# Kernel tuning notes

Hardware: AMD Instinct MI355X
Metric: run time of the kernel (lower is better)

Reference implementation:

```python
import jax, jax.numpy as jnp
import numpy as np

B, S, H = 1, 2048, 2048
NH, NKV, HD = 16, 2, 128
ROPE_THETA = 1000000.0
BF16 = jnp.bfloat16


def setup_inputs() -> dict:
    key = jax.random.key(0)
    ks = jax.random.split(key, 6)
    hidden_states = jax.random.normal(ks[0], (B, S, H), dtype=jnp.float32)
    # causal additive mask, 0 on/below diagonal, large negative above
    causal = jnp.tril(jnp.ones((S, S), dtype=bool))
    attention_mask = jnp.where(causal, 0.0, -1e9).astype(jnp.float32)[None, None, :, :]
    position_ids = jnp.arange(S, dtype=jnp.int32)[None, :]
    sc = 1.0 / np.sqrt(H)
    Wq = jax.random.normal(ks[1], (H, H), dtype=jnp.float32) * sc
    bq = jnp.zeros((H,), dtype=jnp.float32)
    Wk = jax.random.normal(ks[2], (H, NKV * HD), dtype=jnp.float32) * sc
    bk = jnp.zeros((NKV * HD,), dtype=jnp.float32)
    Wv = jax.random.normal(ks[3], (H, NKV * HD), dtype=jnp.float32) * sc
    bv = jnp.zeros((NKV * HD,), dtype=jnp.float32)
    Wo = jax.random.normal(ks[4], (H, H), dtype=jnp.float32) * sc
    return {"hidden_states": hidden_states, "attention_mask": attention_mask,
            "position_ids": position_ids, "Wq": Wq, "bq": bq, "Wk": Wk, "bk": bk,
            "Wv": Wv, "bv": bv, "Wo": Wo}


def _rope_tables(pos):
    # pos: [S] int. freqs: [HD//2]
    freqs = 1.0 / (ROPE_THETA ** (jnp.arange(0, HD, 2, dtype=jnp.float32) / HD))
    ang = pos.astype(jnp.float32)[:, None] * freqs[None, :]  # [S, HD//2]
    return jnp.cos(ang), jnp.sin(ang)


def _apply_rope(x, cos, sin):
    # x: [B,S,nheads,HD]; cos/sin: [S,HD//2] -> broadcast over heads
    c = cos[None, :, None, :]
    s = sin[None, :, None, :]
    x1, x2 = x[..., : HD // 2], x[..., HD // 2 :]
    return jnp.concatenate([x1 * c - x2 * s, x1 * s + x2 * c], axis=-1)


def reference(hidden_states, attention_mask, position_ids, Wq, bq, Wk, bk, Wv, bv, Wo):
    x = hidden_states.astype(BF16)
    # bf16 projections (flax Dense dtype=bfloat16)
    q = (x @ Wq.astype(BF16) + bq.astype(BF16)).reshape(B, S, NH, HD)
    k = (x @ Wk.astype(BF16) + bk.astype(BF16)).reshape(B, S, NKV, HD)
    v = (x @ Wv.astype(BF16) + bv.astype(BF16)).reshape(B, S, NKV, HD)
    cos, sin = _rope_tables(position_ids[0])
    q = _apply_rope(q.astype(jnp.float32), cos, sin).astype(jnp.float32)
    k = _apply_rope(k.astype(jnp.float32), cos, sin).astype(jnp.float32)
    cache_k, cache_v = k, v  # cache holds un-repeated kv (k post-rope, v bf16)
    rep = NH // NKV  # GQA repeat
    k = jnp.repeat(k, rep, axis=2)
    vr = jnp.repeat(v, rep, axis=2)
    # [B,NH,S,HD]
    qh = q.transpose(0, 2, 1, 3)
    kh = k.transpose(0, 2, 1, 3)
    vh = vr.transpose(0, 2, 1, 3).astype(jnp.float32)
    scale = 1.0 / jnp.sqrt(jnp.float32(HD))
    scores = jnp.einsum('bhqd,bhkd->bhqk', qh, kh) * scale + attention_mask
    probs = jnp.clip(jax.nn.softmax(scores.astype(jnp.float32), axis=-1), 1e-09, 1 - 1e-09)
    attn = jnp.einsum('bhqk,bhkd->bhqd', probs, vh)
    attn = attn.transpose(0, 2, 1, 3).reshape(B, S, H)
    out = (attn.astype(BF16) @ Wo.astype(BF16)).astype(jnp.float32)
    return out, cache_k, cache_v
```

## Files before the change

### kernel.cpp

```cpp
#include <hip/hip_runtime.h>
#include <hip/hip_bf16.h>
#include <math.h>

#define S_LEN 2048
#define HDIM  2048
#define N_H   16
#define N_KV  2
#define HD_   128
#define NQKV  2560

typedef __attribute__((ext_vector_type(8))) short bf16x8;
typedef __attribute__((ext_vector_type(4))) float f32x4;
typedef __attribute__((ext_vector_type(16))) float f32x16;

#define GLDS16(gsrc, ldst)                                                      \
  __builtin_amdgcn_global_load_lds(                                             \
      (const __attribute__((address_space(1))) void*)(gsrc),                    \
      (__attribute__((address_space(3))) void*)(ldst), 16, 0, 0)

__device__ __forceinline__ ushort f2b(float x) {
  union { __hip_bfloat16 b; ushort u; } c;
  c.b = __float2bfloat16(x);
  return c.u;
}
__device__ __forceinline__ float b2f(ushort u) {
  union { float f; unsigned v; } c;
  c.v = ((unsigned)u) << 16;
  return c.f;
}
__device__ __forceinline__ uint pk2(float a, float b) {
  return (uint)f2b(a) | ((uint)f2b(b) << 16);
}

__global__ __launch_bounds__(256) void k_prep(const float* __restrict__ hidden,
                                              const float* __restrict__ Wq,
                                              const float* __restrict__ Wk,
                                              const float* __restrict__ Wv,
                                              ushort* __restrict__ x_b,
                                              ushort* __restrict__ wt) {
  __shared__ float t[64][65];
  const int bid = blockIdx.x;
  const int tid = threadIdx.x;
  if (bid < 4096) {
    const int i = bid * 256 + tid;
    float4 v = ((const float4*)hidden)[i];
    ushort4 o;
    o.x = f2b(v.x); o.y = f2b(v.y); o.z = f2b(v.z); o.w = f2b(v.w);
    ((ushort4*)x_b)[i] = o;
    return;
  }
  int tb = bid - 4096;
  const float* src;
  ushort* dst;
  int C, bx, by;
  if (tb < 1024) {
    src = Wq; dst = wt; C = 2048; bx = tb & 31; by = tb >> 5;
  } else if (tb < 1152) {
    tb -= 1024; src = Wk; dst = wt + (size_t)2048 * 2048; C = 256; bx = tb & 3; by = tb >> 2;
  } else {
    tb -= 1152; src = Wv; dst = wt + (size_t)2304 * 2048; C = 256; bx = tb & 3; by = tb >> 2;
  }
  const int c0 = bx * 64, r0 = by * 64;
  const int tx = tid & 63, ty = tid >> 6;
#pragma unroll
  for (int i = 0; i < 16; ++i)
    t[i * 4 + ty][tx] = src[(size_t)(r0 + i * 4 + ty) * C + (c0 + tx)];
  __syncthreads();
#pragma unroll
  for (int i = 0; i < 16; ++i)
    dst[(size_t)(c0 + i * 4 + ty) * 2048 + (r0 + tx)] = f2b(t[tx][i * 4 + ty]);
}

__global__ __launch_bounds__(256) void k_transpose_bf16(const float* __restrict__ src,
                                                        ushort* __restrict__ dst,
                                                        int R, int C) {
  __shared__ float t[64][65];
  int c0 = blockIdx.x * 64, r0 = blockIdx.y * 64;
  int tx = threadIdx.x & 63, ty = threadIdx.x >> 6;
#pragma unroll
  for (int i = 0; i < 16; ++i)
    t[i * 4 + ty][tx] = src[(size_t)(r0 + i * 4 + ty) * C + (c0 + tx)];
  __syncthreads();
#pragma unroll
  for (int i = 0; i < 16; ++i)
    dst[(size_t)(c0 + i * 4 + ty) * R + (r0 + tx)] = f2b(t[tx][i * 4 + ty]);
}

__global__ __launch_bounds__(256) void k_gemm_bt(const ushort* __restrict__ A,
                                                 const ushort* __restrict__ Bt,
                                                 ushort* __restrict__ Cp,
                                                 int M, int N, int Kfull, int Khalf) {
  __shared__ ushort lA[128 * 64];
  __shared__ ushort lB[128 * 64];
  const int tid = threadIdx.x;
  const int w = tid >> 6, lane = tid & 63;
  const int lr = lane & 15, lg = lane >> 4;
  const int bm = blockIdx.x * 128, bn = blockIdx.y * 128;
  const int wm = (w >> 1) * 64, wn = (w & 1) * 64;
  const int kbeg = blockIdx.z * Khalf;
  ushort* Cout = Cp + (size_t)blockIdx.z * M * N;
  f32x4 acc[4][4] = {};

  for (int k0 = kbeg; k0 < kbeg + Khalf; k0 += 64) {
    __syncthreads();
#pragma unroll
    for (int it = 0; it < 4; ++it) {
      const int idx = it * 256 + tid;
      const int row = idx >> 3;
      const int gsl = (idx & 7) ^ (row & 7);
      GLDS16(A + (size_t)(bm + row) * Kfull + k0 + gsl * 8,
             lA + (it * 256 + w * 64) * 8);
      GLDS16(Bt + (size_t)(bn + row) * Kfull + k0 + gsl * 8,
             lB + (it * 256 + w * 64) * 8);
    }
    __syncthreads();
#pragma unroll
    for (int ks = 0; ks < 2; ++ks) {
      bf16x8 af[4], bf[4];
#pragma unroll
      for (int i = 0; i < 4; ++i) {
        const int ra = wm + i * 16 + lr;
        af[i] = *(const bf16x8*)(lA + ra * 64 + (((ks * 4 + lg) ^ (ra & 7)) * 8));
        const int rb = wn + i * 16 + lr;
        bf[i] = *(const bf16x8*)(lB + rb * 64 + (((ks * 4 + lg) ^ (rb & 7)) * 8));
      }
      __builtin_amdgcn_s_setprio(1);
#pragma unroll
      for (int mi = 0; mi < 4; ++mi)
#pragma unroll
        for (int ni = 0; ni < 4; ++ni)
          acc[mi][ni] =
              __builtin_amdgcn_mfma_f32_16x16x32_bf16(af[mi], bf[ni], acc[mi][ni], 0, 0, 0);
      __builtin_amdgcn_s_setprio(0);
    }
  }

#pragma unroll
  for (int mi = 0; mi < 4; ++mi)
#pragma unroll
    for (int ni = 0; ni < 4; ++ni)
#pragma unroll
      for (int r = 0; r < 4; ++r) {
        const int row = bm + wm + mi * 16 + lg * 4 + r;
        const int col = bn + wn + ni * 16 + lr;
        Cout[(size_t)row * N + col] = f2b(acc[mi][ni][r]);
      }
}

__global__ __launch_bounds__(256) void k_epirope(const ushort* __restrict__ p0,
                                                 const ushort* __restrict__ p1,
                                                 const float* __restrict__ bq,
                                                 const float* __restrict__ bk,
                                                 const float* __restrict__ bv,
                                                 const int* __restrict__ pos_ids,
                                                 ushort* __restrict__ q_r,
                                                 ushort* __restrict__ k_r,
                                                 ushort* __restrict__ v_t,
                                                 float* __restrict__ cache_k,
                                                 float* __restrict__ cache_v) {
  const int s = blockIdx.x;
  const int t = threadIdx.x;
  __shared__ float row[NQKV];
  const uint* a = (const uint*)(p0 + (size_t)s * NQKV);
  const uint* b = (const uint*)(p1 + (size_t)s * NQKV);
#pragma unroll
  for (int j = 0; j < 5; ++j) {
    const int c2 = t + 256 * j;
    const uint u0 = a[c2], u1 = b[c2];
    const int c = 2 * c2;
    const float v0 = b2f((ushort)u0) + b2f((ushort)(u1 & 0xffff));
    const float v1 = b2f((ushort)(u0 >> 16)) + b2f((ushort)(u1 >> 16));
    const float bias0 = (c < 2048) ? bq[c] : (c < 2304 ? bk[c - 2048] : bv[c - 2304]);
    const float bias1 = (c + 1 < 2048) ? bq[c + 1]
                                       : (c + 1 < 2304 ? bk[c + 1 - 2048] : bv[c + 1 - 2304]);
    row[c] = b2f(f2b(b2f(f2b(v0)) + b2f(f2b(bias0))));
    row[c + 1] = b2f(f2b(b2f(f2b(v1)) + b2f(f2b(bias1))));
  }
  __syncthreads();

  const int i = t & 63, g = t >> 6;
  const float SCALE = 0.08838834764831845f;
  const float pos = (float)pos_ids[s];
  const float freq = (float)(1.0 / pow(1000000.0, (double)i / 64.0));
  float sn, cs;
  sincosf(pos * freq, &sn, &cs);

#pragma unroll
  for (int j = 0; j < 4; ++j) {
    const int h = j * 4 + g;
    const float x1 = row[h * 128 + i];
    const float x2 = row[h * 128 + 64 + i];
    const float o1 = x1 * cs - x2 * sn;
    const float o2 = x1 * sn + x2 * cs;
    const size_t qo = ((size_t)h * S_LEN + s) * 128;
    q_r[qo + i] = f2b(o1 * SCALE);
    q_r[qo + 64 + i] = f2b(o2 * SCALE);
  }
  if (g < 2) {
    const int kv = g;
    const float x1 = row[2048 + kv * 128 + i];
    const float x2 = row[2048 + kv * 128 + 64 + i];
    const float o1 = x1 * cs - x2 * sn;
    const float o2 = x1 * sn + x2 * cs;
    const size_t ko = ((size_t)kv * S_LEN + s) * 128;
    k_r[ko + i] = f2b(o1);
    k_r[ko + 64 + i] = f2b(o2);
    const size_t co = ((size_t)s * 2 + kv) * 128;
    cache_k[co + i] = o1;
    cache_k[co + 64 + i] = o2;
  }
  {
    const int kv = t >> 7, d = t & 127;
    const float vval = row[2304 + kv * 128 + d];
    cache_v[((size_t)s * 2 + kv) * 128 + d] = vval;
    v_t[((size_t)kv * 128 + d) * S_LEN + s] = f2b(vval);
  }
}

__global__ __launch_bounds__(256) void k_addround(const ushort* __restrict__ p0,
                                                  const ushort* __restrict__ p1,
                                                  float* __restrict__ out, int n2) {
  int i = blockIdx.x * 256 + threadIdx.x;
  if (i >= n2) return;
  const uint a = ((const uint*)p0)[i];
  const uint b = ((const uint*)p1)[i];
  float2 o;
  o.x = b2f(f2b(b2f((ushort)(a & 0xffff)) + b2f((ushort)(b & 0xffff))));
  o.y = b2f(f2b(b2f((ushort)(a >> 16)) + b2f((ushort)(b >> 16))));
  ((float2*)out)[i] = o;
}

__global__ __launch_bounds__(256, 2) void k_attn(const ushort* __restrict__ q_r,
                                                 const ushort* __restrict__ k_r,
                                                 const ushort* __restrict__ v_t,
                                                 ushort* __restrict__ attn_b) {
  __shared__ ushort smem[2][2][8192];
  __shared__ float stats[2][32][2];

  const int bi = blockIdx.x;
  const int h = bi & 15;
  const int tq = (bi >> 4) & 15;
  const int Q = (bi >> 8) ? (31 - tq) : tq;
  const int kvh = h >> 3;

  const int tid = threadIdx.x, w = tid >> 6, lane = tid & 63;
  const int g = w >> 1, wq = w & 1, tg = tid & 127;
  const int l31 = lane & 31, hb = lane >> 5;
  const int S_steps = Q + 1;
  const int qmaxw = Q * 64 + wq * 32 + 31;

  bf16x8 qf[8];
  {
    const ushort* qp =
        q_r + ((size_t)(h * S_LEN + Q * 64 + wq * 32 + l31)) * 128 + hb * 8;
#pragma unroll
    for (int f = 0; f < 8; ++f) qf[f] = *(const bf16x8*)(qp + f * 16);
  }

  f32x16 acc[4] = {};
  float m = -INFINITY, l = 0.f;

#define STAGE(BUF, T32)                                                           \
  do {                                                                            \
    const int kb_ = (T32) * 32;                                                   \
    _Pragma("unroll") for (int i = 0; i < 4; ++i) {                               \
      const int idx = i * 128 + tg;                                               \
      {                                                                           \
        const int key = idx >> 4, sl = idx & 15;                                  \
        GLDS16(k_r + ((size_t)(kvh * S_LEN + kb_ + key)) * 128 +                  \
                   ((sl ^ (key & 7)) * 8),                                        \
               &smem[g][BUF][i * 1024 + wq * 512]);                               \
      }                                                                           \
      {                                                                           \
        const int d = idx >> 2, p = idx & 3;                                      \
        const int gs = (p - (d >> 1)) & 3;                                        \
        GLDS16(v_t + ((size_t)(kvh * HD_ + d)) * S_LEN + kb_ + gs * 8,            \
               &smem[g][BUF][4096 + i * 1024 + wq * 512]);                        \
      }                                                                           \
    }                                                                             \
  } while (0)

  STAGE(0, g);
  int buf = 0;

  for (int s = 0; s < S_steps; ++s) {
    __syncthreads();
    if (s + 1 < S_steps) STAGE(buf ^ 1, 2 * (s + 1) + g);
    const int kb = (2 * s + g) * 32;

    if (kb <= qmaxw) {
      const ushort* lK = &smem[g][buf][0];
      const ushort* lV = &smem[g][buf][4096];

      f32x16 p0 = {};
      __builtin_amdgcn_s_setprio(1);
#pragma unroll
      for (int f = 0; f < 8; ++f) {
        const int key = l31;
        const bf16x8 kf8 =
            *(const bf16x8*)(lK + key * 128 + (((2 * f + hb) ^ (key & 7)) * 8));
        p0 = __builtin_amdgcn_mfma_f32_32x32x16_bf16(kf8, qf[f], p0, 0, 0, 0);
      }
      __builtin_amdgcn_s_setprio(0);

      const int q = Q * 64 + wq * 32 + l31;
      float sv[16];
#pragma unroll
      for (int r = 0; r < 16; ++r) {
        const int key = kb + (r & 3) + 8 * (r >> 2) + 4 * hb;
        sv[r] = (key <= q) ? p0[r] : -INFINITY;
      }
      float t8[8];
#pragma unroll
      for (int j = 0; j < 8; ++j) t8[j] = fmaxf(sv[j], sv[j + 8]);
#pragma unroll
      for (int st = 4; st >= 1; st >>= 1)
#pragma unroll
        for (int j = 0; j < 4; ++j)
          if (j < st) t8[j] = fmaxf(t8[j], t8[j + st]);
      const float mxw = fmaxf(t8[0], __shfl_xor(t8[0], 32));

      if (__any(mxw > m + 8.f)) {
        const float mn = fmaxf(m, mxw);
        const float sc = __expf(m - mn);
#pragma unroll
        for (int g2 = 0; g2 < 4; ++g2)
#pragma unroll
          for (int r = 0; r < 16; ++r) acc[g2][r] *= sc;
        l *= sc;
        m = mn;
      }
#pragma unroll
      for (int r = 0; r < 16; ++r) sv[r] = __expf(sv[r] - m);
      float ts[8];
#pragma unroll
      for (int j = 0; j < 8; ++j) ts[j] = sv[j] + sv[j + 8];
#pragma unroll
      for (int st = 4; st >= 1; st >>= 1)
#pragma unroll
        for (int j = 0; j < 4; ++j)
          if (j < st) ts[j] += ts[j + st];
      l += ts[0];

      uint pk8[8];
#pragma unroll
      for (int j = 0; j < 8; ++j) pk8[j] = pk2(sv[2 * j], sv[2 * j + 1]);
      union FragU { uint wd[4]; bf16x8 v; };
      FragU frag[2];
#pragma unroll
      for (int c1 = 0; c1 < 2; ++c1) {
        uint mine0, mine1, rcv0, rcv1;
        {
          const uint pa_ = pk8[0 + 4 * c1];
          const uint pb_ = pk8[2 + 4 * c1];
          const uint mn_ = hb ? pb_ : pa_;
          const uint xc_ = hb ? pa_ : pb_;
          mine0 = mn_;
          rcv0 = (uint)__shfl_xor((int)xc_, 32);
        }
        {
          const uint pa_ = pk8[1 + 4 * c1];
          const uint pb_ = pk8[3 + 4 * c1];
          const uint mn_ = hb ? pb_ : pa_;
          const uint xc_ = hb ? pa_ : pb_;
          mine1 = mn_;
          rcv1 = (uint)__shfl_xor((int)xc_, 32);
        }
        frag[c1].wd[0] = hb ? rcv0 : mine0;
        frag[c1].wd[1] = hb ? rcv1 : mine1;
        frag[c1].wd[2] = hb ? mine0 : rcv0;
        frag[c1].wd[3] = hb ? mine1 : rcv1;
      }

      __builtin_amdgcn_s_setprio(1);
#pragma unroll
      for (int g2 = 0; g2 < 4; ++g2) {
        const int d = g2 * 32 + l31;
#pragma unroll
        for (int c = 0; c < 2; ++c) {
          const int phys = ((2 * c + hb) + (d >> 1)) & 3;
          const bf16x8 vf = *(const bf16x8*)(lV + d * 32 + phys * 8);
          acc[g2] = __builtin_amdgcn_mfma_f32_32x32x16_bf16(vf, frag[c].v, acc[g2], 0, 0, 0);
        }
      }
      __builtin_amdgcn_s_setprio(0);
    }
    buf ^= 1;
  }
  __syncthreads();

  float* mrg = (float*)&smem[0][0][0];
  float* ldsO = (float*)&smem[1][0][0];
  if (g == 1) {
    const float lt1 = l + __shfl_xor(l, 32);
#pragma unroll
    for (int g2 = 0; g2 < 4; ++g2)
#pragma unroll
      for (int r = 0; r < 16; ++r) {
        const int d5 = (r & 3) + 8 * (r >> 2) + 4 * hb;
        mrg[wq * 4096 + (g2 * 32 + d5) * 32 + l31] = acc[g2][r];
      }
    if (hb == 0) {
      stats[wq][l31][0] = m;
      stats[wq][l31][1] = lt1;
    }
  }
  __syncthreads();
  if (g == 0) {
    const float m1 = stats[wq][l31][0];
    const float l1 = stats[wq][l31][1];
    const float l0 = l + __shfl_xor(l, 32);
    const float ms = fmaxf(m, m1);
    const float f0 = __expf(m - ms);
    const float f1 = __expf(m1 - ms);
    const float inv = 1.0f / (l0 * f0 + l1 * f1);
#pragma unroll
    for (int g2 = 0; g2 < 4; ++g2)
#pragma unroll
      for (int r = 0; r < 16; ++r) {
        const int d5 = (r & 3) + 8 * (r >> 2) + 4 * hb;
        const float o1v = mrg[wq * 4096 + (g2 * 32 + d5) * 32 + l31];
        const float val = (acc[g2][r] * f0 + o1v * f1) * inv;
        ldsO[wq * 4096 + l31 * 128 + g2 * 32 + (d5 ^ l31)] = val;
      }
#pragma unroll
    for (int pass = 0; pass < 8; ++pass) {
      const int qrow = pass * 4 + (lane >> 4);
      const int d0 = (lane & 15) * 8;
      float v[8];
#pragma unroll
      for (int j = 0; j < 8; ++j)
        v[j] = ldsO[wq * 4096 + qrow * 128 + (((d0 + j) & 31) ^ qrow) + (d0 & 96)];
      uint4 o;
      o.x = pk2(v[0], v[1]); o.y = pk2(v[2], v[3]);
      o.z = pk2(v[4], v[5]); o.w = pk2(v[6], v[7]);
      const size_t qg = (size_t)(Q * 64 + wq * 32 + qrow);
      *(uint4*)(attn_b + qg * HDIM + h * 128 + d0) = o;
    }
  }
#undef STAGE
}

extern "C" void kernel_launch(void* const* d_in, const int* in_sizes, int n_in,
                              void* d_out, int out_size, void* d_ws, size_t ws_size,
                              hipStream_t stream) {
  const float* hidden = (const float*)d_in[0];
  const int* pos_ids = (const int*)d_in[2];
  const float* Wq = (const float*)d_in[3];
  const float* bq = (const float*)d_in[4];
  const float* Wk = (const float*)d_in[5];
  const float* bk = (const float*)d_in[6];
  const float* Wv = (const float*)d_in[7];
  const float* bv = (const float*)d_in[8];
  const float* Wo = (const float*)d_in[9];

  float* out = (float*)d_out;
  float* cache_k = out + (size_t)S_LEN * HDIM;
  float* cache_v = cache_k + (size_t)S_LEN * N_KV * HD_;

  char* ws = (char*)d_ws;
  ushort* x_b = (ushort*)(ws);
  ushort* wt = (ushort*)(ws + (8ull << 20));
  ushort* qkvp = (ushort*)(ws + (18ull << 20));
  ushort* q_r = (ushort*)(ws);
  ushort* k_r = (ushort*)(ws + (8ull << 20));
  ushort* v_t = (ushort*)(ws + (9ull << 20));
  ushort* wo_t = (ushort*)(ws + (10ull << 20));
  ushort* attn_b = (ushort*)(ws + (18ull << 20));
  ushort* outp = (ushort*)(ws + (26ull << 20));

  k_prep<<<dim3(5376), 256, 0, stream>>>(hidden, Wq, Wk, Wv, x_b, wt);
  k_gemm_bt<<<dim3(16, 20, 2), 256, 0, stream>>>(x_b, wt, qkvp, 2048, 2560, 2048, 1024);
  k_transpose_bf16<<<dim3(32, 32), 256, 0, stream>>>(Wo, wo_t, 2048, 2048);
  k_epirope<<<dim3(S_LEN), 256, 0, stream>>>(qkvp, qkvp + (size_t)2048 * 2560, bq, bk, bv,
                                             pos_ids, q_r, k_r, v_t, cache_k, cache_v);
  k_attn<<<dim3(512), 256, 0, stream>>>(q_r, k_r, v_t, attn_b);
  k_gemm_bt<<<dim3(16, 16, 2), 256, 0, stream>>>(attn_b, wo_t, outp, 2048, 2048, 2048, 1024);
  k_addround<<<dim3((2048 * 2048 / 2 + 255) / 256), 256, 0, stream>>>(
      outp, outp + (size_t)2048 * 2048, out, 2048 * 2048 / 2);
}
```

Baseline: 142.1 us.

## Split attention KV range across four waves per 32-query tile, load K/V directly

The attention kernel now assigns each block a 32-query tile and splits the key range across four waves, with each wave reading K and V fragments straight from global memory instead of staging them through double-buffered LDS. The four partial softmax states are merged through LDS, with partial outputs stored as bf16, and the grid doubles to 1024 blocks. This removes the per-step block barriers and LDS staging and adds parallelism for short causal tiles. In exchange it relies on cache hits for repeated K/V reads, and rounding the partials to bf16 adds error. The RoPE frequency is also computed with a float exp2 instead of a double-precision pow.

```diff
diff --git a/kernel.cpp b/kernel.cpp
--- a/kernel.cpp
+++ b/kernel.cpp
@@ -181,7 +181,7 @@
   const int i = t & 63, g = t >> 6;
   const float SCALE = 0.08838834764831845f;
   const float pos = (float)pos_ids[s];
-  const float freq = (float)(1.0 / pow(1000000.0, (double)i / 64.0));
+  const float freq = exp2f(-0.31143075889569023f * (float)i);
   float sn, cs;
   sincosf(pos * freq, &sn, &cs);
 
@@ -230,29 +230,28 @@
   ((float2*)out)[i] = o;
 }
 
-__global__ __launch_bounds__(256, 2) void k_attn(const ushort* __restrict__ q_r,
-                                                 const ushort* __restrict__ k_r,
-                                                 const ushort* __restrict__ v_t,
-                                                 ushort* __restrict__ attn_b) {
-  __shared__ ushort smem[2][2][8192];
-  __shared__ float stats[2][32][2];
+__global__ __launch_bounds__(256) void k_attn(const ushort* __restrict__ q_r,
+                                              const ushort* __restrict__ k_r,
+                                              const ushort* __restrict__ v_t,
+                                              ushort* __restrict__ attn_b) {
+  __shared__ ushort pb[4][4096];
+  __shared__ float sm[4][32], sl[4][32];
+  __shared__ float w4[32][4];
 
   const int bi = blockIdx.x;
   const int h = bi & 15;
-  const int tq = (bi >> 4) & 15;
-  const int Q = (bi >> 8) ? (31 - tq) : tq;
+  const int t6 = (bi >> 4) & 31;
+  const int Q32 = (bi >> 9) ? (63 - t6) : t6;
   const int kvh = h >> 3;
 
-  const int tid = threadIdx.x, w = tid >> 6, lane = tid & 63;
-  const int g = w >> 1, wq = w & 1, tg = tid & 127;
+  const int tid = threadIdx.x, p = tid >> 6, lane = tid & 63;
   const int l31 = lane & 31, hb = lane >> 5;
-  const int S_steps = Q + 1;
-  const int qmaxw = Q * 64 + wq * 32 + 31;
+  const int qglob = Q32 * 32 + l31;
+  const int qmax = Q32 * 32 + 31;
 
   bf16x8 qf[8];
   {
-    const ushort* qp =
-        q_r + ((size_t)(h * S_LEN + Q * 64 + wq * 32 + l31)) * 128 + hb * 8;
+    const ushort* qp = q_r + ((size_t)(h * S_LEN + qglob)) * 128 + hb * 8;
 #pragma unroll
     for (int f = 0; f < 8; ++f) qf[f] = *(const bf16x8*)(qp + f * 16);
   }
@@ -260,185 +259,157 @@
   f32x16 acc[4] = {};
   float m = -INFINITY, l = 0.f;
 
-#define STAGE(BUF, T32)                                                           \
-  do {                                                                            \
-    const int kb_ = (T32) * 32;                                                   \
-    _Pragma("unroll") for (int i = 0; i < 4; ++i) {                               \
-      const int idx = i * 128 + tg;                                               \
-      {                                                                           \
-        const int key = idx >> 4, sl = idx & 15;                                  \
-        GLDS16(k_r + ((size_t)(kvh * S_LEN + kb_ + key)) * 128 +                  \
-                   ((sl ^ (key & 7)) * 8),                                        \
-               &smem[g][BUF][i * 1024 + wq * 512]);                               \
-      }                                                                           \
-      {                                                                           \
-        const int d = idx >> 2, p = idx & 3;                                      \
-        const int gs = (p - (d >> 1)) & 3;                                        \
-        GLDS16(v_t + ((size_t)(kvh * HD_ + d)) * S_LEN + kb_ + gs * 8,            \
-               &smem[g][BUF][4096 + i * 1024 + wq * 512]);                        \
-      }                                                                           \
-    }                                                                             \
-  } while (0)
-
-  STAGE(0, g);
-  int buf = 0;
-
-  for (int s = 0; s < S_steps; ++s) {
-    __syncthreads();
-    if (s + 1 < S_steps) STAGE(buf ^ 1, 2 * (s + 1) + g);
-    const int kb = (2 * s + g) * 32;
-
-    if (kb <= qmaxw) {
-      const ushort* lK = &smem[g][buf][0];
-      const ushort* lV = &smem[g][buf][4096];
-
-      f32x16 p0 = {};
+  const ushort* Kb = k_r + (size_t)kvh * S_LEN * 128;
+  const ushort* Vb = v_t + (size_t)kvh * HD_ * S_LEN;
+
+  for (int t = p; t * 32 <= qmax; t += 4) {
+    const int kb = t * 32;
+    const ushort* kRow = Kb + (size_t)(kb + l31) * 128;
+
+    f32x16 p0 = {};
+    {
+      bf16x8 kf[4];
+#pragma unroll
+      for (int f = 0; f < 4; ++f) kf[f] = *(const bf16x8*)(kRow + (2 * f + hb) * 8);
       __builtin_amdgcn_s_setprio(1);
 #pragma unroll
-      for (int f = 0; f < 8; ++f) {
-        const int key = l31;
-        const bf16x8 kf8 =
-            *(const bf16x8*)(lK + key * 128 + (((2 * f + hb) ^ (key & 7)) * 8));
-        p0 = __builtin_amdgcn_mfma_f32_32x32x16_bf16(kf8, qf[f], p0, 0, 0, 0);
-      }
+      for (int f = 0; f < 4; ++f)
+        p0 = __builtin_amdgcn_mfma_f32_32x32x16_bf16(kf[f], qf[f], p0, 0, 0, 0);
       __builtin_amdgcn_s_setprio(0);
-
-      const int q = Q * 64 + wq * 32 + l31;
-      float sv[16];
+#pragma unroll
+      for (int f = 0; f < 4; ++f) kf[f] = *(const bf16x8*)(kRow + (2 * f + 8 + hb) * 8);
+      __builtin_amdgcn_s_setprio(1);
+#pragma unroll
+      for (int f = 0; f < 4; ++f)
+        p0 = __builtin_amdgcn_mfma_f32_32x32x16_bf16(kf[f], qf[f + 4], p0, 0, 0, 0);
+      __builtin_amdgcn_s_setprio(0);
+    }
+
+    float sv[16];
+#pragma unroll
+    for (int r = 0; r < 16; ++r) {
+      const int key = kb + (r & 3) + 8 * (r >> 2) + 4 * hb;
+      sv[r] = (key <= qglob) ? p0[r] : -INFINITY;
+    }
+    float t8[8];
+#pragma unroll
+    for (int j = 0; j < 8; ++j) t8[j] = fmaxf(sv[j], sv[j + 8]);
+#pragma unroll
+    for (int st = 4; st >= 1; st >>= 1)
+#pragma unroll
+      for (int j = 0; j < 4; ++j)
+        if (j < st) t8[j] = fmaxf(t8[j], t8[j + st]);
+    const float mxw = fmaxf(t8[0], __shfl_xor(t8[0], 32));
+
+    if (__any(mxw > m + 8.f)) {
+      const float mn = fmaxf(m, mxw);
+      const float sc = __expf(m - mn);
+#pragma unroll
+      for (int g2 = 0; g2 < 4; ++g2)
+#pragma unroll
+        for (int r = 0; r < 16; ++r) acc[g2][r] *= sc;
+      l *= sc;
+      m = mn;
+    }
+#pragma unroll
+    for (int r = 0; r < 16; ++r) sv[r] = __expf(sv[r] - m);
+    float ts[8];
+#pragma unroll
+    for (int j = 0; j < 8; ++j) ts[j] = sv[j] + sv[j + 8];
+#pragma unroll
+    for (int st = 4; st >= 1; st >>= 1)
+#pragma unroll
+      for (int j = 0; j < 4; ++j)
+        if (j < st) ts[j] += ts[j + st];
+    l += ts[0];
+
+    uint pk8[8];
+#pragma unroll
+    for (int j = 0; j < 8; ++j) pk8[j] = pk2(sv[2 * j], sv[2 * j + 1]);
+    union FragU { uint wd[4]; bf16x8 v; };
+    FragU frag[2];
+#pragma unroll
+    for (int c1 = 0; c1 < 2; ++c1) {
+      uint mine0, mine1, rcv0, rcv1;
+      {
+        const uint pa_ = pk8[0 + 4 * c1];
+        const uint pb_ = pk8[2 + 4 * c1];
+        const uint mn_ = hb ? pb_ : pa_;
+        const uint xc_ = hb ? pa_ : pb_;
+        mine0 = mn_;
+        rcv0 = (uint)__shfl_xor((int)xc_, 32);
+      }
+      {
+        const uint pa_ = pk8[1 + 4 * c1];
+        const uint pb_ = pk8[3 + 4 * c1];
+        const uint mn_ = hb ? pb_ : pa_;
+        const uint xc_ = hb ? pa_ : pb_;
+        mine1 = mn_;
+        rcv1 = (uint)__shfl_xor((int)xc_, 32);
+      }
+      frag[c1].wd[0] = hb ? rcv0 : mine0;
+      frag[c1].wd[1] = hb ? rcv1 : mine1;
+      frag[c1].wd[2] = hb ? mine0 : rcv0;
+      frag[c1].wd[3] = hb ? mine1 : rcv1;
+    }
+
+    __builtin_amdgcn_s_setprio(1);
+#pragma unroll
+    for (int g2 = 0; g2 < 4; ++g2) {
+      const int d = g2 * 32 + l31;
+      const ushort* vRow = Vb + (size_t)d * S_LEN + kb;
+#pragma unroll
+      for (int c = 0; c < 2; ++c) {
+        const bf16x8 vf = *(const bf16x8*)(vRow + (2 * c + hb) * 8);
+        acc[g2] = __builtin_amdgcn_mfma_f32_32x32x16_bf16(vf, frag[c].v, acc[g2], 0, 0, 0);
+      }
+    }
+    __builtin_amdgcn_s_setprio(0);
+  }
+
+  {
+    const float lt = l + __shfl_xor(l, 32);
+#pragma unroll
+    for (int g2 = 0; g2 < 4; ++g2)
 #pragma unroll
       for (int r = 0; r < 16; ++r) {
-        const int key = kb + (r & 3) + 8 * (r >> 2) + 4 * hb;
-        sv[r] = (key <= q) ? p0[r] : -INFINITY;
-      }
-      float t8[8];
-#pragma unroll
-      for (int j = 0; j < 8; ++j) t8[j] = fmaxf(sv[j], sv[j + 8]);
-#pragma unroll
-      for (int st = 4; st >= 1; st >>= 1)
-#pragma unroll
-        for (int j = 0; j < 4; ++j)
-          if (j < st) t8[j] = fmaxf(t8[j], t8[j + st]);
-      const float mxw = fmaxf(t8[0], __shfl_xor(t8[0], 32));
-
-      if (__any(mxw > m + 8.f)) {
-        const float mn = fmaxf(m, mxw);
-        const float sc = __expf(m - mn);
-#pragma unroll
-        for (int g2 = 0; g2 < 4; ++g2)
-#pragma unroll
-          for (int r = 0; r < 16; ++r) acc[g2][r] *= sc;
-        l *= sc;
-        m = mn;
-      }
-#pragma unroll
-      for (int r = 0; r < 16; ++r) sv[r] = __expf(sv[r] - m);
-      float ts[8];
-#pragma unroll
-      for (int j = 0; j < 8; ++j) ts[j] = sv[j] + sv[j + 8];
-#pragma unroll
-      for (int st = 4; st >= 1; st >>= 1)
-#pragma unroll
-        for (int j = 0; j < 4; ++j)
-          if (j < st) ts[j] += ts[j + st];
-      l += ts[0];
-
-      uint pk8[8];
-#pragma unroll
-      for (int j = 0; j < 8; ++j) pk8[j] = pk2(sv[2 * j], sv[2 * j + 1]);
-      union FragU { uint wd[4]; bf16x8 v; };
-      FragU frag[2];
-#pragma unroll
-      for (int c1 = 0; c1 < 2; ++c1) {
-        uint mine0, mine1, rcv0, rcv1;
-        {
-          const uint pa_ = pk8[0 + 4 * c1];
-          const uint pb_ = pk8[2 + 4 * c1];
-          const uint mn_ = hb ? pb_ : pa_;
-          const uint xc_ = hb ? pa_ : pb_;
-          mine0 = mn_;
-          rcv0 = (uint)__shfl_xor((int)xc_, 32);
-        }
-        {
-          const uint pa_ = pk8[1 + 4 * c1];
-          const uint pb_ = pk8[3 + 4 * c1];
-          const uint mn_ = hb ? pb_ : pa_;
-          const uint xc_ = hb ? pa_ : pb_;
-          mine1 = mn_;
-          rcv1 = (uint)__shfl_xor((int)xc_, 32);
-        }
-        frag[c1].wd[0] = hb ? rcv0 : mine0;
-        frag[c1].wd[1] = hb ? rcv1 : mine1;
-        frag[c1].wd[2] = hb ? mine0 : rcv0;
-        frag[c1].wd[3] = hb ? mine1 : rcv1;
-      }
-
-      __builtin_amdgcn_s_setprio(1);
-#pragma unroll
-      for (int g2 = 0; g2 < 4; ++g2) {
-        const int d = g2 * 32 + l31;
-#pragma unroll
-        for (int c = 0; c < 2; ++c) {
-          const int phys = ((2 * c + hb) + (d >> 1)) & 3;
-          const bf16x8 vf = *(const bf16x8*)(lV + d * 32 + phys * 8);
-          acc[g2] = __builtin_amdgcn_mfma_f32_32x32x16_bf16(vf, frag[c].v, acc[g2], 0, 0, 0);
-        }
-      }
-      __builtin_amdgcn_s_setprio(0);
-    }
-    buf ^= 1;
+        const int d = g2 * 32 + (r & 3) + 8 * (r >> 2) + 4 * hb;
+        pb[p][l31 * 128 + (d ^ ((l31 & 15) << 3))] = f2b(acc[g2][r]);
+      }
+    sm[p][l31] = m;
+    sl[p][l31] = lt;
   }
   __syncthreads();
-
-  float* mrg = (float*)&smem[0][0][0];
-  float* ldsO = (float*)&smem[1][0][0];
-  if (g == 1) {
-    const float lt1 = l + __shfl_xor(l, 32);
-#pragma unroll
-    for (int g2 = 0; g2 < 4; ++g2)
-#pragma unroll
-      for (int r = 0; r < 16; ++r) {
-        const int d5 = (r & 3) + 8 * (r >> 2) + 4 * hb;
-        mrg[wq * 4096 + (g2 * 32 + d5) * 32 + l31] = acc[g2][r];
-      }
-    if (hb == 0) {
-      stats[wq][l31][0] = m;
-      stats[wq][l31][1] = lt1;
-    }
+  {
+    const int q = l31;
+    float mm[4], ll[4];
+#pragma unroll
+    for (int pp = 0; pp < 4; ++pp) { mm[pp] = sm[pp][q]; ll[pp] = sl[pp][q]; }
+    const float ms = fmaxf(fmaxf(mm[0], mm[1]), fmaxf(mm[2], mm[3]));
+    float wv[4], L = 0.f;
+#pragma unroll
+    for (int pp = 0; pp < 4; ++pp) {
+      wv[pp] = __expf(mm[pp] - ms);
+      L += ll[pp] * wv[pp];
+    }
+    const float inv = 1.0f / L;
+    if (p == 0 && hb == 0)
+#pragma unroll
+      for (int pp = 0; pp < 4; ++pp) w4[q][pp] = wv[pp] * inv;
   }
   __syncthreads();
-  if (g == 0) {
-    const float m1 = stats[wq][l31][0];
-    const float l1 = stats[wq][l31][1];
-    const float l0 = l + __shfl_xor(l, 32);
-    const float ms = fmaxf(m, m1);
-    const float f0 = __expf(m - ms);
-    const float f1 = __expf(m1 - ms);
-    const float inv = 1.0f / (l0 * f0 + l1 * f1);
-#pragma unroll
-    for (int g2 = 0; g2 < 4; ++g2)
-#pragma unroll
-      for (int r = 0; r < 16; ++r) {
-        const int d5 = (r & 3) + 8 * (r >> 2) + 4 * hb;
-        const float o1v = mrg[wq * 4096 + (g2 * 32 + d5) * 32 + l31];
-        const float val = (acc[g2][r] * f0 + o1v * f1) * inv;
-        ldsO[wq * 4096 + l31 * 128 + g2 * 32 + (d5 ^ l31)] = val;
-      }
-#pragma unroll
-    for (int pass = 0; pass < 8; ++pass) {
-      const int qrow = pass * 4 + (lane >> 4);
-      const int d0 = (lane & 15) * 8;
-      float v[8];
-#pragma unroll
-      for (int j = 0; j < 8; ++j)
-        v[j] = ldsO[wq * 4096 + qrow * 128 + (((d0 + j) & 31) ^ qrow) + (d0 & 96)];
-      uint4 o;
-      o.x = pk2(v[0], v[1]); o.y = pk2(v[2], v[3]);
-      o.z = pk2(v[4], v[5]); o.w = pk2(v[6], v[7]);
-      const size_t qg = (size_t)(Q * 64 + wq * 32 + qrow);
-      *(uint4*)(attn_b + qg * HDIM + h * 128 + d0) = o;
-    }
-  }
-#undef STAGE
+  {
+    const int d = p * 32 + l31;
+#pragma unroll
+    for (int j = 0; j < 16; ++j) {
+      const int q = (j & 3) + 8 * (j >> 2) + 4 * hb;
+      const float4 wq = *(const float4*)&w4[q][0];
+      const int idx = q * 128 + (d ^ ((q & 15) << 3));
+      float val = b2f(pb[0][idx]) * wq.x + b2f(pb[1][idx]) * wq.y +
+                  b2f(pb[2][idx]) * wq.z + b2f(pb[3][idx]) * wq.w;
+      attn_b[(size_t)(Q32 * 32 + q) * HDIM + h * 128 + d] = f2b(val);
+    }
+  }
 }
 
 extern "C" void kernel_launch(void* const* d_in, const int* in_sizes, int n_in,
@@ -474,7 +445,7 @@
   k_transpose_bf16<<<dim3(32, 32), 256, 0, stream>>>(Wo, wo_t, 2048, 2048);
   k_epirope<<<dim3(S_LEN), 256, 0, stream>>>(qkvp, qkvp + (size_t)2048 * 2560, bq, bk, bv,
                                              pos_ids, q_r, k_r, v_t, cache_k, cache_v);
-  k_attn<<<dim3(512), 256, 0, stream>>>(q_r, k_r, v_t, attn_b);
+  k_attn<<<dim3(1024), 256, 0, stream>>>(q_r, k_r, v_t, attn_b);
   k_gemm_bt<<<dim3(16, 16, 2), 256, 0, stream>>>(attn_b, wo_t, outp, 2048, 2048, 2048, 1024);
   k_addround<<<dim3((2048 * 2048 / 2 + 255) / 256), 256, 0, stream>>>(
       outp, outp + (size_t)2048 * 2048, out, 2048 * 2048 / 2);
```

Result: slower. 156.0 us (+9.8%).
